# Kernel optimization log

Hardware: AMD Instinct MI355X
Metric: run time of the kernel (lower is better)

The kernel has to match this reference:

```python
import jax, jax.numpy as jnp
import numpy as np

T, C, H, E, TOPK = 8192, 1024, 4096, 8, 2
ALPHA = 0.01


def setup_inputs() -> dict:
    key = jax.random.key(0)
    ks = jax.random.split(key, 10)
    std = 0.01
    return {
        "x": jax.random.normal(ks[0], (T, C), dtype=jnp.float32),
        "gate_w": jax.random.normal(ks[1], (E, C), dtype=jnp.float32) * std,  # nn.init.normal_(std=0.01)
        "wg": jax.random.normal(ks[2], (E, C, H), dtype=jnp.float32) * 0.02,
        "wu": jax.random.normal(ks[3], (E, C, H), dtype=jnp.float32) * 0.02,
        "wd": jax.random.normal(ks[4], (E, H, C), dtype=jnp.float32) * 0.02,
        "swg": jax.random.normal(ks[5], (C, H), dtype=jnp.float32) * 0.02,
        "swu": jax.random.normal(ks[6], (C, H), dtype=jnp.float32) * 0.02,
        "swd": jax.random.normal(ks[7], (H, C), dtype=jnp.float32) * 0.02,
        "shared_scale": jnp.ones((1,), dtype=jnp.float32) * 0.5,
    }


def _swiglu(h, g, u, d):
    # SwiGLU FFN: W_down( silu(W_gate x) * W_up x )
    return (jax.nn.silu(h @ g) * (h @ u)) @ d


def reference(x, gate_w, wg, wu, wd, swg, swu, swd, shared_scale):
    # ---- gate (top-k softmax routing) ----
    logits = x @ gate_w.T                       # [T, E]
    scores = jax.nn.softmax(logits, axis=-1)    # [T, E]
    topk_w, topk_idx = jax.lax.top_k(scores, TOPK)
    topk_w = topk_w / jnp.sum(topk_w, axis=-1, keepdims=True)

    # per-token combine weight for each expert: sum_k w_k * [idx_k == e]  -> [T, E]
    comb = jnp.zeros((x.shape[0], E), dtype=x.dtype)
    comb = comb.at[jnp.arange(x.shape[0])[:, None], topk_idx].add(topk_w)

    # ---- routed experts (dispatch-FFN-combine, expressed as masked dense combine) ----
    y = jnp.zeros_like(x)
    for e in range(E):  # fixed small expert count
        y = y + comb[:, e:e + 1] * _swiglu(x, wg[e], wu[e], wd[e])

    # ---- shared expert ----
    y = y + shared_scale * _swiglu(x, swg, swu, swd)

    # ---- load-balancing aux loss (training mode) ----
    onehot = jax.nn.one_hot(topk_idx.reshape(-1), E, dtype=x.dtype)  # [T*K, E]
    ce = onehot.mean(axis=0)
    fi = ce * E
    Pi = scores.mean(axis=0)
    aux_loss = jnp.sum(Pi * fi) * ALPHA
    return y, aux_loss
```

## Files before the change

kernel.cpp:

```cpp
#include <hip/hip_runtime.h>
#include <hip/hip_bf16.h>
#include <stdint.h>

#define T_TOK 8192
#define CDIM  1024
#define HDIM  4096
#define NEXP  8
#define TOPK_ 2
#define GT_MAX 72
#define UT_MAX 104
#define GROWS_MAX (GT_MAX * 256)

typedef __attribute__((ext_vector_type(8))) short short8;
typedef __attribute__((ext_vector_type(4))) float f32x4;

__device__ __forceinline__ void gload16(const short* g, short* l) {
  __builtin_amdgcn_global_load_lds(
      (const __attribute__((address_space(1))) unsigned int*)(g),
      (__attribute__((address_space(3))) unsigned int*)(l), 16, 0, 0);
}

__global__ __launch_bounds__(256) void gate_kernel(
    const float* __restrict__ x, const float* __restrict__ gw,
    int* __restrict__ tokinfo, float* __restrict__ tokw,
    int* __restrict__ bcnt, float* __restrict__ spart)
{
  const int wid = threadIdx.x >> 6, lane = threadIdx.x & 63;
  const int t = blockIdx.x * 4 + wid;
  float acc[NEXP];
#pragma unroll
  for (int e = 0; e < NEXP; ++e) acc[e] = 0.f;
  const float4* xr = (const float4*)x + (size_t)t * (CDIM / 4);
  const float4* gw4 = (const float4*)gw;
#pragma unroll
  for (int i = 0; i < CDIM / 256; ++i) {
    const float4 xv = xr[lane + 64 * i];
#pragma unroll
    for (int e = 0; e < NEXP; ++e) {
      const float4 gv = gw4[e * (CDIM / 4) + lane + 64 * i];
      acc[e] += xv.x * gv.x + xv.y * gv.y + xv.z * gv.z + xv.w * gv.w;
    }
  }
#pragma unroll
  for (int off = 32; off > 0; off >>= 1) {
#pragma unroll
    for (int e = 0; e < NEXP; ++e) acc[e] += __shfl_xor(acc[e], off);
  }
  float mx = acc[0];
#pragma unroll
  for (int e = 1; e < NEXP; ++e) mx = fmaxf(mx, acc[e]);
  float p[NEXP]; float s = 0.f;
#pragma unroll
  for (int e = 0; e < NEXP; ++e) { p[e] = __expf(acc[e] - mx); s += p[e]; }
  const float inv = 1.f / s;
#pragma unroll
  for (int e = 0; e < NEXP; ++e) p[e] *= inv;
  float v0 = p[0]; int i0 = 0;
#pragma unroll
  for (int e = 1; e < NEXP; ++e) if (p[e] > v0) { v0 = p[e]; i0 = e; }
  float v1 = -1.f; int i1 = 0;
#pragma unroll
  for (int e = 0; e < NEXP; ++e) if (e != i0 && p[e] > v1) { v1 = p[e]; i1 = e; }

  __shared__ float sp[4][NEXP];
  __shared__ int   se[4][2];
  __shared__ float swt[4][2];
  if (lane == 0) {
#pragma unroll
    for (int e = 0; e < NEXP; ++e) sp[wid][e] = p[e];
    const float wn = 1.f / (v0 + v1);
    se[wid][0] = i0; se[wid][1] = i1;
    swt[wid][0] = v0 * wn; swt[wid][1] = v1 * wn;
  }
  __syncthreads();
  if (threadIdx.x == 0) {
    int cnt[NEXP];
#pragma unroll
    for (int e = 0; e < NEXP; ++e) cnt[e] = 0;
#pragma unroll
    for (int tt = 0; tt < 4; ++tt) {
      const int e0 = se[tt][0], e1 = se[tt][1];
      const int r0 = cnt[e0]++; const int r1 = cnt[e1]++;
      tokinfo[blockIdx.x * 4 + tt] = e0 | (e1 << 3) | (r0 << 6) | (r1 << 10);
      ((float2*)tokw)[blockIdx.x * 4 + tt] = make_float2(swt[tt][0], swt[tt][1]);
    }
#pragma unroll
    for (int e = 0; e < NEXP; ++e) bcnt[blockIdx.x * NEXP + e] = cnt[e];
  }
  if (threadIdx.x < NEXP)
    spart[blockIdx.x * NEXP + threadIdx.x] =
        sp[0][threadIdx.x] + sp[1][threadIdx.x] + sp[2][threadIdx.x] + sp[3][threadIdx.x];
}

__global__ __launch_bounds__(512) void scan_kernel(
    const int* __restrict__ bcnt, int* __restrict__ boff, int* __restrict__ ecnt,
    const float* __restrict__ spart, float* __restrict__ aux_out,
    int* __restrict__ pad_off, int* __restrict__ tile_map, int* __restrict__ ntiles)
{
  const int w = threadIdx.x >> 6, l = threadIdx.x & 63;
  int run = 0;
#pragma unroll 4
  for (int c = 0; c < (T_TOK / 4) / 64; ++c) {
    const int b = c * 64 + l;
    const int v = bcnt[b * NEXP + w];
    int sc = v;
#pragma unroll
    for (int off = 1; off < 64; off <<= 1) {
      const int t = __shfl_up(sc, off);
      if (l >= off) sc += t;
    }
    boff[b * NEXP + w] = run + sc - v;
    run += __shfl(sc, 63);
  }
  if (l == 0) ecnt[w] = run;
  float fs = 0.f;
  for (int c = 0; c < (T_TOK / 4) / 64; ++c) fs += spart[(c * 64 + l) * NEXP + w];
#pragma unroll
  for (int off = 32; off > 0; off >>= 1) fs += __shfl_xor(fs, off);
  __shared__ float pis[NEXP];
  __shared__ int cs[NEXP];
  if (l == 0) { pis[w] = fs; cs[w] = run; }
  __syncthreads();
  if (threadIdx.x == 0) {
    float aux = 0.f;
#pragma unroll
    for (int e = 0; e < NEXP; ++e) {
      const float Pi = pis[e] / (float)T_TOK;
      const float ce = (float)cs[e] / (float)(T_TOK * TOPK_);
      aux += Pi * ce * (float)NEXP;
    }
    aux_out[0] = aux * 0.01f;
    ecnt[8] = T_TOK;
    int acc = 0, nt = 0;
    for (int e = 0; e < NEXP; ++e) {
      pad_off[e] = acc;
      const int te = (cs[e] + 255) >> 8;
      for (int t = 0; t < te; ++t) { tile_map[nt] = e | ((t * 256) << 4); ++nt; }
      acc += te * 256;
    }
    ntiles[0] = nt;
    for (int t = 0; t < T_TOK / 256; ++t) { tile_map[nt] = 8 | ((t * 256) << 4); ++nt; }
    ntiles[1] = nt;
  }
}

__global__ __launch_bounds__(256) void scatter_kernel(
    const int* __restrict__ tokinfo, const float* __restrict__ tokw,
    const int* __restrict__ boff, const int* __restrict__ pad_off,
    int* __restrict__ grows, float* __restrict__ gww, int2* __restrict__ tokpos)
{
  const int t = blockIdx.x * 256 + threadIdx.x;
  const int info = tokinfo[t];
  const int e0 = info & 7, e1 = (info >> 3) & 7;
  const int r0 = (info >> 6) & 15, r1 = (info >> 10) & 15;
  const int b = t >> 2;
  const float2 wv = ((const float2*)tokw)[t];
  const int g0 = pad_off[e0] + boff[b * NEXP + e0] + r0;
  grows[g0] = t; gww[g0] = wv.x;
  const int g1 = pad_off[e1] + boff[b * NEXP + e1] + r1;
  grows[g1] = t; gww[g1] = wv.y;
  tokpos[t] = make_int2(g0, g1);
}

__global__ __launch_bounds__(256) void cvt_x_kernel(const float* __restrict__ x,
                                                    __hip_bfloat16* __restrict__ xb)
{
  const int i = blockIdx.x * 256 + threadIdx.x;
  const float4 v = ((const float4*)x)[i];
  union { __hip_bfloat16 h[4]; uint2 u; } o;
  o.h[0] = __float2bfloat16(v.x); o.h[1] = __float2bfloat16(v.y);
  o.h[2] = __float2bfloat16(v.z); o.h[3] = __float2bfloat16(v.w);
  ((uint2*)xb)[i] = o.u;
}

struct TD { const float* src; __hip_bfloat16* dst; int N; int nsh; int M; };
struct TB { TD d[27]; };
__global__ __launch_bounds__(256) void tbatch_kernel(TB tb)
{
  const int m = blockIdx.x >> 12;
  const int t = blockIdx.x & 4095;
  const TD td = tb.d[m];
  const int n0 = (t & ((1 << td.nsh) - 1)) << 5;
  const int m0 = (t >> td.nsh) << 5;
  __shared__ float tile[32][33];
  const int tx = threadIdx.x & 31, ty = threadIdx.x >> 5;
#pragma unroll
  for (int i = 0; i < 4; ++i)
    tile[ty + 8 * i][tx] = td.src[(size_t)(m0 + ty + 8 * i) * td.N + n0 + tx];
  __syncthreads();
#pragma unroll
  for (int i = 0; i < 4; ++i)
    td.dst[(size_t)(n0 + ty + 8 * i) * td.M + m0 + tx] = __float2bfloat16(tile[tx][ty + 8 * i]);
}

__global__ __launch_bounds__(512, 2) void gemm1_pipe_kernel(
    const __hip_bfloat16* __restrict__ Abase,
    const __hip_bfloat16* __restrict__ B0mat, const __hip_bfloat16* __restrict__ B1mat,
    __hip_bfloat16* __restrict__ midout,
    const int* __restrict__ rowlist, const int* __restrict__ ecnt,
    const int* __restrict__ tile_map, const int* __restrict__ ntiles,
    int mode, int tile_base)
{
  constexpr int K = CDIM;
  constexpr int NT = 32;
  __shared__ __align__(16) short lds[65536];

  int ti = blockIdx.y + tile_base;
  if (mode == 2) ti += ntiles[0];
  const int hi = (mode == 1) ? ntiles[0] : ntiles[1];
  if (ti >= hi) return;
  const int tm = tile_map[ti];
  const int e = tm & 15, rb = tm >> 4;
  const int rows_valid = ecnt[e] - rb;
  const int gbmid = (int)blockIdx.y * 256;
  const int glist = ti * 256;

  const int t = threadIdx.x, l = t & 63, w = t >> 6;
  const int sr = t >> 2;
  const int csrc = (t & 3) ^ ((t >> 3) & 3);
  const int n0 = blockIdx.x * 128;

  int r0g, r1g;
  if (e == 8) { r0g = rb + sr; r1g = rb + 128 + sr; }
  else {
    const int c0 = sr < rows_valid ? sr : rows_valid - 1;
    const int c1 = (128 + sr) < rows_valid ? (128 + sr) : rows_valid - 1;
    r0g = rowlist[glist + c0]; r1g = rowlist[glist + c1];
  }
  const short* pA0 = (const short*)Abase + (size_t)r0g * K + csrc * 8;
  const short* pA1 = (const short*)Abase + (size_t)r1g * K + csrc * 8;
  const int br0 = sr, br1 = 128 + sr;
  const int s0 = (br0 >> 4) & 1, s1 = (br1 >> 4) & 1;
  const int h0 = n0 + (br0 >> 5) * 16 + (br0 & 15);
  const int h1 = n0 + (br1 >> 5) * 16 + (br1 & 15);
  const short* pB0 = (const short*)(s0 ? B1mat : B0mat) + (size_t)e * CDIM * HDIM + (size_t)h0 * K + csrc * 8;
  const short* pB1 = (const short*)(s1 ? B1mat : B0mat) + (size_t)e * CDIM * HDIM + (size_t)h1 * K + csrc * 8;

  short* dstA = lds + w * 512;
  short* dstB = lds + 32768 + w * 512;

  const int wr = w >> 2, wc = w & 3;
  const int chunk = (((l >> 4) ^ ((l >> 1) & 3)) << 3);
  const int afb = wr * 4096 + (l & 15) * 32 + chunk;
  const int bfb = 32768 + (wc >> 1) * 4096 + ((wc & 1) * 64 + (l & 15)) * 32 + chunk;

  f32x4 acc[8][4];
#pragma unroll
  for (int i = 0; i < 8; ++i)
#pragma unroll
    for (int j = 0; j < 4; ++j) acc[i][j] = (f32x4){0.f, 0.f, 0.f, 0.f};

#define STAGE_A(q) { const int s8_ = ((q) & 3) * 8192; \
    gload16(pA0 + (q) * 32, dstA + s8_); \
    gload16(pA1 + (q) * 32, dstA + s8_ + 4096); }
#define STAGE_B(q) { const int s8_ = ((q) & 3) * 8192; \
    gload16(pB0 + (q) * 32, dstB + s8_); \
    gload16(pB1 + (q) * 32, dstB + s8_ + 4096); }

  STAGE_A(0) STAGE_B(0) STAGE_A(1) STAGE_B(1)

  short8 af[8], bf[4];
  for (int q = 0; q < NT; ++q) {
    const int s8 = (q & 3) * 8192;
    if (q == NT - 1) {
      asm volatile("s_waitcnt vmcnt(0)\n\ts_barrier" ::: "memory");
    } else {
      asm volatile("s_waitcnt vmcnt(4)\n\ts_barrier" ::: "memory");
    }
    __builtin_amdgcn_sched_barrier(0);
    if (q + 2 < NT) STAGE_A(q + 2)
#pragma unroll
    for (int mi = 0; mi < 4; ++mi) af[mi] = *(const short8*)(lds + s8 + afb + mi * 512);
#pragma unroll
    for (int ni = 0; ni < 4; ++ni) bf[ni] = *(const short8*)(lds + s8 + bfb + ni * 512);
#pragma unroll
    for (int mi = 4; mi < 8; ++mi) af[mi] = *(const short8*)(lds + s8 + afb + mi * 512);
    __builtin_amdgcn_s_setprio(1);
#pragma unroll
    for (int mi = 0; mi < 4; ++mi)
#pragma unroll
      for (int ni = 0; ni < 4; ++ni)
        acc[mi][ni] = __builtin_amdgcn_mfma_f32_16x16x32_bf16(af[mi], bf[ni], acc[mi][ni], 0, 0, 0);
    __builtin_amdgcn_s_setprio(0);
    if (q + 2 < NT) STAGE_B(q + 2)
    __builtin_amdgcn_s_setprio(1);
#pragma unroll
    for (int mi = 4; mi < 8; ++mi)
#pragma unroll
      for (int ni = 0; ni < 4; ++ni)
        acc[mi][ni] = __builtin_amdgcn_mfma_f32_16x16x32_bf16(af[mi], bf[ni], acc[mi][ni], 0, 0, 0);
    __builtin_amdgcn_s_setprio(0);
  }
#undef STAGE_A
#undef STAGE_B

  const int rl = (l >> 4) * 4, cl = l & 15;
#pragma unroll
  for (int mi = 0; mi < 8; ++mi) {
#pragma unroll
    for (int j = 0; j < 4; ++j) {
      const int rlocal = wr * 128 + mi * 16 + rl + j;
      if (rlocal < rows_valid) {
        __hip_bfloat16* mp = midout + (size_t)(gbmid + rlocal) * HDIM;
#pragma unroll
        for (int jj = 0; jj < 2; ++jj) {
          const float g = acc[mi][jj * 2][j], u = acc[mi][jj * 2 + 1][j];
          const float sv = g / (1.f + __expf(-g));
          mp[n0 + (wc * 2 + jj) * 16 + cl] = __float2bfloat16(sv * u);
        }
      }
    }
  }
}

template <int OST>
__global__ __launch_bounds__(512, 1) void gemm2_pipe_kernel(
    const __hip_bfloat16* __restrict__ mid, const __hip_bfloat16* __restrict__ wd9,
    float* __restrict__ mid2, float* __restrict__ y,
    const int* __restrict__ rowlist, const float* __restrict__ roww,
    const int* __restrict__ ecnt, const int* __restrict__ tile_map,
    const int* __restrict__ ntiles, const float* __restrict__ ssc,
    int mode, int tile_base)
{
  constexpr int K = HDIM;
  constexpr int NT = K / 32;
  __shared__ __align__(16) short lds[49152];

  int ti = blockIdx.y + tile_base;
  if (mode == 2) ti += ntiles[0];
  const int hi = (mode == 1) ? ntiles[0] : ntiles[1];
  if (ti >= hi) return;
  const int tm = tile_map[ti];
  const int e = tm & 15, rb = tm >> 4;
  const int rows_valid = ecnt[e] - rb;
  const int gbmid = (int)blockIdx.y * 256;
  const int glist = ti * 256;

  const int t = threadIdx.x, l = t & 63, w = t >> 6;
  const int sr = t >> 2;
  const int csrc = (t & 3) ^ ((t >> 3) & 3);
  const int n0 = blockIdx.x * 128;

  const short* pA0 = (const short*)mid + (size_t)(gbmid + sr) * K + csrc * 8;
  const short* pA1 = pA0 + (size_t)128 * K;
  const short* pB0 = (const short*)wd9 + (size_t)e * CDIM * HDIM + (size_t)(n0 + sr) * K + csrc * 8;

  short* dA = lds + w * 512;
  short* dB = lds + 32768 + w * 512;

  const int wr = w >> 2, wc = w & 3;
  const int chunk = (((l >> 4) ^ ((l >> 1) & 3)) << 3);
  const int afb = wr * 4096 + (l & 15) * 32 + chunk;
  const int bfb = 32768 + (wc * 32 + (l & 15)) * 32 + chunk;

  f32x4 acc[8][2];
#pragma unroll
  for (int i = 0; i < 8; ++i) { acc[i][0] = (f32x4){0.f,0.f,0.f,0.f}; acc[i][1] = (f32x4){0.f,0.f,0.f,0.f}; }

#define S_A(q) { const int o_ = ((q) & 3) * 8192; \
    gload16(pA0 + (size_t)(q) * 32, dA + o_); \
    gload16(pA1 + (size_t)(q) * 32, dA + o_ + 4096); }
#define S_B(q) { const int o_ = ((q) & 3) * 4096; \
    gload16(pB0 + (size_t)(q) * 32, dB + o_); }

  S_A(0) S_B(0) S_A(1) S_B(1)

  short8 af[8], bf[2];
  for (int q = 0; q < NT; ++q) {
    const int sA = (q & 3) * 8192, sB = (q & 3) * 4096;
    if (q == NT - 1) {
      asm volatile("s_waitcnt vmcnt(0)\n\ts_barrier" ::: "memory");
    } else {
      asm volatile("s_waitcnt vmcnt(3)\n\ts_barrier" ::: "memory");
    }
    __builtin_amdgcn_sched_barrier(0);
    if (q + 2 < NT) { S_A(q + 2) S_B(q + 2) }
#pragma unroll
    for (int mi = 0; mi < 8; ++mi) af[mi] = *(const short8*)(lds + sA + afb + mi * 512);
    bf[0] = *(const short8*)(lds + sB + bfb);
    bf[1] = *(const short8*)(lds + sB + bfb + 512);
    __builtin_amdgcn_s_setprio(1);
#pragma unroll
    for (int mi = 0; mi < 8; ++mi) {
      acc[mi][0] = __builtin_amdgcn_mfma_f32_16x16x32_bf16(af[mi], bf[0], acc[mi][0], 0, 0, 0);
      acc[mi][1] = __builtin_amdgcn_mfma_f32_16x16x32_bf16(af[mi], bf[1], acc[mi][1], 0, 0, 0);
    }
    __builtin_amdgcn_s_setprio(0);
  }
#undef S_A
#undef S_B

  const int rl = (l >> 4) * 4, cl = l & 15;
  if (OST) {
#pragma unroll
    for (int mi = 0; mi < 8; ++mi) {
#pragma unroll
      for (int j = 0; j < 4; ++j) {
        const int rlocal = wr * 128 + mi * 16 + rl + j;
        if (rlocal < rows_valid) {
          float* mp = mid2 + (size_t)(glist + rlocal) * CDIM + n0 + wc * 32 + cl;
          mp[0]  = acc[mi][0][j];
          mp[16] = acc[mi][1][j];
        }
      }
    }
  } else {
    const float ss = ssc[0];
#pragma unroll
    for (int mi = 0; mi < 8; ++mi) {
#pragma unroll
      for (int j = 0; j < 4; ++j) {
        const int rlocal = wr * 128 + mi * 16 + rl + j;
        if (rlocal < rows_valid) {
          int tok; float wgt;
          if (e == 8) { tok = rb + rlocal; wgt = ss; }
          else { tok = rowlist[glist + rlocal]; wgt = roww[glist + rlocal]; }
          float* yp = y + (size_t)tok * CDIM + n0 + wc * 32 + cl;
          unsafeAtomicAdd(yp,      wgt * acc[mi][0][j]);
          unsafeAtomicAdd(yp + 16, wgt * acc[mi][1][j]);
        }
      }
    }
  }
}

__global__ __launch_bounds__(256) void combine_kernel(
    const float* __restrict__ mid2, const int* __restrict__ ntiles,
    const int2* __restrict__ tokpos, const float* __restrict__ tokw,
    const float* __restrict__ ssc, float* __restrict__ y)
{
  const int t = blockIdx.x;
  const int c = threadIdx.x * 4;
  const int dbase = ntiles[0] * 256;
  const int2 gp = tokpos[t];
  const float2 wv = ((const float2*)tokw)[t];
  const float ss = ssc[0];
  const float4 d = *(const float4*)(mid2 + (size_t)(dbase + t) * CDIM + c);
  const float4 a = *(const float4*)(mid2 + (size_t)gp.x * CDIM + c);
  const float4 b = *(const float4*)(mid2 + (size_t)gp.y * CDIM + c);
  float4 r;
  r.x = ss * d.x + wv.x * a.x + wv.y * b.x;
  r.y = ss * d.y + wv.x * a.y + wv.y * b.y;
  r.z = ss * d.z + wv.x * a.z + wv.y * b.z;
  r.w = ss * d.w + wv.x * a.w + wv.y * b.w;
  *(float4*)(y + (size_t)t * CDIM + c) = r;
}

extern "C" void kernel_launch(void* const* d_in, const int* in_sizes, int n_in,
                              void* d_out, int out_size, void* d_ws, size_t ws_size,
                              hipStream_t stream)
{
  const float* x   = (const float*)d_in[0];
  const float* gw  = (const float*)d_in[1];
  const float* wg  = (const float*)d_in[2];
  const float* wu  = (const float*)d_in[3];
  const float* wd  = (const float*)d_in[4];
  const float* swg = (const float*)d_in[5];
  const float* swu = (const float*)d_in[6];
  const float* swd = (const float*)d_in[7];
  const float* ssc = (const float*)d_in[8];
  float* y = (float*)d_out;

  auto al = [](size_t v) { return (v + 255) & ~(size_t)255; };
  char* ws = (char*)d_ws;
  size_t off = 0;
  __hip_bfloat16* xb = (__hip_bfloat16*)(ws + off); off += al((size_t)T_TOK * CDIM * 2);
  int*   tokinfo = (int*)(ws + off);   off += al((size_t)T_TOK * 4);
  float* tokw    = (float*)(ws + off); off += al((size_t)T_TOK * 8);
  int2*  tokpos  = (int2*)(ws + off);  off += al((size_t)T_TOK * 8);
  int*   bcnt    = (int*)(ws + off);   off += al((size_t)(T_TOK / 4) * NEXP * 4);
  int*   boffb   = (int*)(ws + off);   off += al((size_t)(T_TOK / 4) * NEXP * 4);
  float* spart   = (float*)(ws + off); off += al((size_t)(T_TOK / 4) * NEXP * 4);
  int*   ecnt    = (int*)(ws + off);   off += 256;
  int*   pad_off = (int*)(ws + off);   off += 256;
  int*   ntiles  = (int*)(ws + off);   off += 256;
  int*   tile_map= (int*)(ws + off);   off += al((size_t)UT_MAX * 4);
  int*   grows   = (int*)(ws + off);   off += al((size_t)GROWS_MAX * 4);
  float* gww     = (float*)(ws + off); off += al((size_t)GROWS_MAX * 4);

  const size_t WMAT = (size_t)CDIM * HDIM;
  __hip_bfloat16* wg9 = (__hip_bfloat16*)(ws + off); off += 9 * WMAT * 2;
  __hip_bfloat16* wu9 = (__hip_bfloat16*)(ws + off); off += 9 * WMAT * 2;
  __hip_bfloat16* wd9 = (__hip_bfloat16*)(ws + off); off += 9 * WMAT * 2;
  __hip_bfloat16* mid = (__hip_bfloat16*)(ws + off);
  const size_t mid_avail = (ws_size > off) ? (ws_size - off) : 0;
  const size_t TILE_B = (size_t)256 * HDIM * 2;
  const size_t MIDB   = (size_t)UT_MAX * TILE_B;
  const size_t MID2B  = (size_t)UT_MAX * 256 * CDIM * 4;

  gate_kernel<<<T_TOK / 4, 256, 0, stream>>>(x, gw, tokinfo, tokw, bcnt, spart);
  scan_kernel<<<1, 512, 0, stream>>>(bcnt, boffb, ecnt, spart, y + (size_t)T_TOK * CDIM,
                                     pad_off, tile_map, ntiles);
  scatter_kernel<<<T_TOK / 256, 256, 0, stream>>>(tokinfo, tokw, boffb, pad_off,
                                                  grows, gww, tokpos);
  cvt_x_kernel<<<T_TOK * CDIM / 4 / 256, 256, 0, stream>>>(x, xb);

  TB tb;
  for (int e = 0; e < 8; ++e) {
    tb.d[e]      = TD{wg + e * WMAT, wg9 + e * WMAT, HDIM, 7, CDIM};
    tb.d[8 + e]  = TD{wu + e * WMAT, wu9 + e * WMAT, HDIM, 7, CDIM};
    tb.d[16 + e] = TD{wd + e * WMAT, wd9 + e * WMAT, CDIM, 5, HDIM};
  }
  tb.d[24] = TD{swg, wg9 + 8 * WMAT, HDIM, 7, CDIM};
  tb.d[25] = TD{swu, wu9 + 8 * WMAT, HDIM, 7, CDIM};
  tb.d[26] = TD{swd, wd9 + 8 * WMAT, CDIM, 5, HDIM};
  tbatch_kernel<<<27 * 4096, 256, 0, stream>>>(tb);

  if (mid_avail >= MIDB + MID2B) {
    float* mid2 = (float*)((char*)mid + MIDB);
    gemm1_pipe_kernel<<<dim3(HDIM / 128, UT_MAX), 512, 0, stream>>>(
        xb, wg9, wu9, mid, grows, ecnt, tile_map, ntiles, 0, 0);
    gemm2_pipe_kernel<1><<<dim3(CDIM / 128, UT_MAX), 512, 0, stream>>>(
        mid, wd9, mid2, nullptr, grows, gww, ecnt, tile_map, ntiles, ssc, 0, 0);
    combine_kernel<<<T_TOK, 256, 0, stream>>>(mid2, ntiles, tokpos, tokw, ssc, y);
  } else if (mid_avail >= MIDB) {
    hipMemsetAsync(y, 0, (size_t)T_TOK * CDIM * sizeof(float), stream);
    gemm1_pipe_kernel<<<dim3(HDIM / 128, UT_MAX), 512, 0, stream>>>(
        xb, wg9, wu9, mid, grows, ecnt, tile_map, ntiles, 0, 0);
    gemm2_pipe_kernel<0><<<dim3(CDIM / 128, UT_MAX), 512, 0, stream>>>(
        mid, wd9, nullptr, y, grows, gww, ecnt, tile_map, ntiles, ssc, 0, 0);
  } else {
    hipMemsetAsync(y, 0, (size_t)T_TOK * CDIM * sizeof(float), stream);
    int CH = (int)(mid_avail / TILE_B);
    if (CH < 1) CH = 1;
    for (int c0 = 0; c0 < GT_MAX; c0 += CH) {
      const int g = (GT_MAX - c0) < CH ? (GT_MAX - c0) : CH;
      gemm1_pipe_kernel<<<dim3(HDIM / 128, g), 512, 0, stream>>>(
          xb, wg9, wu9, mid, grows, ecnt, tile_map, ntiles, 1, c0);
      gemm2_pipe_kernel<0><<<dim3(CDIM / 128, g), 512, 0, stream>>>(
          mid, wd9, nullptr, y, grows, gww, ecnt, tile_map, ntiles, ssc, 1, c0);
    }
    for (int c0 = 0; c0 < 32; c0 += CH) {
      const int g = (32 - c0) < CH ? (32 - c0) : CH;
      gemm1_pipe_kernel<<<dim3(HDIM / 128, g), 512, 0, stream>>>(
          xb, wg9, wu9, mid, grows, ecnt, tile_map, ntiles, 2, c0);
      gemm2_pipe_kernel<0><<<dim3(CDIM / 128, g), 512, 0, stream>>>(
          mid, wd9, nullptr, y, grows, gww, ecnt, tile_map, ntiles, ssc, 2, c0);
    }
  }
}
```

Measured before the change: 1.006 ms.

## Fuse x bf16 conversion into gate; rework GEMM pipelines to BK=64 double-buffer

Result: no change. 1.014 ms (+0.8%).

```diff
diff --git a/kernel.cpp b/kernel.cpp
--- a/kernel.cpp
+++ b/kernel.cpp
@@ -23,7 +23,8 @@
 __global__ __launch_bounds__(256) void gate_kernel(
     const float* __restrict__ x, const float* __restrict__ gw,
     int* __restrict__ tokinfo, float* __restrict__ tokw,
-    int* __restrict__ bcnt, float* __restrict__ spart)
+    int* __restrict__ bcnt, float* __restrict__ spart,
+    __hip_bfloat16* __restrict__ xb)
 {
   const int wid = threadIdx.x >> 6, lane = threadIdx.x & 63;
   const int t = blockIdx.x * 4 + wid;
@@ -32,9 +33,14 @@
   for (int e = 0; e < NEXP; ++e) acc[e] = 0.f;
   const float4* xr = (const float4*)x + (size_t)t * (CDIM / 4);
   const float4* gw4 = (const float4*)gw;
+  uint2* xbo = (uint2*)(xb + (size_t)t * CDIM);
 #pragma unroll
   for (int i = 0; i < CDIM / 256; ++i) {
     const float4 xv = xr[lane + 64 * i];
+    union { __hip_bfloat16 h[4]; uint2 u; } o;
+    o.h[0] = __float2bfloat16(xv.x); o.h[1] = __float2bfloat16(xv.y);
+    o.h[2] = __float2bfloat16(xv.z); o.h[3] = __float2bfloat16(xv.w);
+    xbo[lane + 64 * i] = o.u;
 #pragma unroll
     for (int e = 0; e < NEXP; ++e) {
       const float4 gv = gw4[e * (CDIM / 4) + lane + 64 * i];
@@ -162,17 +168,6 @@
   tokpos[t] = make_int2(g0, g1);
 }
 
-__global__ __launch_bounds__(256) void cvt_x_kernel(const float* __restrict__ x,
-                                                    __hip_bfloat16* __restrict__ xb)
-{
-  const int i = blockIdx.x * 256 + threadIdx.x;
-  const float4 v = ((const float4*)x)[i];
-  union { __hip_bfloat16 h[4]; uint2 u; } o;
-  o.h[0] = __float2bfloat16(v.x); o.h[1] = __float2bfloat16(v.y);
-  o.h[2] = __float2bfloat16(v.z); o.h[3] = __float2bfloat16(v.w);
-  ((uint2*)xb)[i] = o.u;
-}
-
 struct TD { const float* src; __hip_bfloat16* dst; int N; int nsh; int M; };
 struct TB { TD d[27]; };
 __global__ __launch_bounds__(256) void tbatch_kernel(TB tb)
@@ -202,7 +197,7 @@
     int mode, int tile_base)
 {
   constexpr int K = CDIM;
-  constexpr int NT = 32;
+  constexpr int NTL = K / 64;
   __shared__ __align__(16) short lds[65536];
 
   int ti = blockIdx.y + tile_base;
@@ -216,33 +211,30 @@
   const int glist = ti * 256;
 
   const int t = threadIdx.x, l = t & 63, w = t >> 6;
-  const int sr = t >> 2;
-  const int csrc = (t & 3) ^ ((t >> 3) & 3);
-  const int n0 = blockIdx.x * 128;
-
-  int r0g, r1g;
-  if (e == 8) { r0g = rb + sr; r1g = rb + 128 + sr; }
-  else {
-    const int c0 = sr < rows_valid ? sr : rows_valid - 1;
-    const int c1 = (128 + sr) < rows_valid ? (128 + sr) : rows_valid - 1;
-    r0g = rowlist[glist + c0]; r1g = rowlist[glist + c1];
-  }
-  const short* pA0 = (const short*)Abase + (size_t)r0g * K + csrc * 8;
-  const short* pA1 = (const short*)Abase + (size_t)r1g * K + csrc * 8;
-  const int br0 = sr, br1 = 128 + sr;
-  const int s0 = (br0 >> 4) & 1, s1 = (br1 >> 4) & 1;
-  const int h0 = n0 + (br0 >> 5) * 16 + (br0 & 15);
-  const int h1 = n0 + (br1 >> 5) * 16 + (br1 & 15);
-  const short* pB0 = (const short*)(s0 ? B1mat : B0mat) + (size_t)e * CDIM * HDIM + (size_t)h0 * K + csrc * 8;
-  const short* pB1 = (const short*)(s1 ? B1mat : B0mat) + (size_t)e * CDIM * HDIM + (size_t)h1 * K + csrc * 8;
-
-  short* dstA = lds + w * 512;
-  short* dstB = lds + 32768 + w * 512;
-
   const int wr = w >> 2, wc = w & 3;
-  const int chunk = (((l >> 4) ^ ((l >> 1) & 3)) << 3);
-  const int afb = wr * 4096 + (l & 15) * 32 + chunk;
-  const int bfb = 32768 + (wc >> 1) * 4096 + ((wc & 1) * 64 + (l & 15)) * 32 + chunk;
+  const int n0h = blockIdx.x * 128;
+
+  const int rbase = w * 8 + (l >> 3);
+  const int ksrc = ((l & 7) ^ ((l >> 3) & 7)) * 8;
+  const short* pA[4]; const short* pB[4];
+#pragma unroll
+  for (int j = 0; j < 4; ++j) {
+    const int rl_ = j * 64 + rbase;
+    int rg;
+    if (e == 8) rg = rb + rl_;
+    else { const int c = rl_ < rows_valid ? rl_ : rows_valid - 1; rg = rowlist[glist + c]; }
+    pA[j] = (const short*)Abase + (size_t)rg * K + ksrc;
+    const int s = (rl_ >> 4) & 1;
+    const int h = n0h + (rl_ >> 5) * 16 + (rl_ & 15);
+    pB[j] = (const short*)(s ? B1mat : B0mat) + (size_t)e * CDIM * HDIM + (size_t)h * K + ksrc;
+  }
+  const int dst0 = w * 512 + l * 8;
+
+#define STG(tt) { const int bb_ = ((tt) & 1) * 16384; \
+    gload16(pA[0] + (tt) * 64, lds + bb_ + dst0);          gload16(pB[0] + (tt) * 64, lds + 32768 + bb_ + dst0); \
+    gload16(pA[1] + (tt) * 64, lds + bb_ + 4096 + dst0);   gload16(pB[1] + (tt) * 64, lds + 32768 + bb_ + 4096 + dst0); \
+    gload16(pA[2] + (tt) * 64, lds + bb_ + 8192 + dst0);   gload16(pB[2] + (tt) * 64, lds + 32768 + bb_ + 8192 + dst0); \
+    gload16(pA[3] + (tt) * 64, lds + bb_ + 12288 + dst0);  gload16(pB[3] + (tt) * 64, lds + 32768 + bb_ + 12288 + dst0); }
 
   f32x4 acc[8][4];
 #pragma unroll
@@ -250,49 +242,33 @@
 #pragma unroll
     for (int j = 0; j < 4; ++j) acc[i][j] = (f32x4){0.f, 0.f, 0.f, 0.f};
 
-#define STAGE_A(q) { const int s8_ = ((q) & 3) * 8192; \
-    gload16(pA0 + (q) * 32, dstA + s8_); \
-    gload16(pA1 + (q) * 32, dstA + s8_ + 4096); }
-#define STAGE_B(q) { const int s8_ = ((q) & 3) * 8192; \
-    gload16(pB0 + (q) * 32, dstB + s8_); \
-    gload16(pB1 + (q) * 32, dstB + s8_ + 4096); }
-
-  STAGE_A(0) STAGE_B(0) STAGE_A(1) STAGE_B(1)
-
-  short8 af[8], bf[4];
-  for (int q = 0; q < NT; ++q) {
-    const int s8 = (q & 3) * 8192;
-    if (q == NT - 1) {
-      asm volatile("s_waitcnt vmcnt(0)\n\ts_barrier" ::: "memory");
-    } else {
-      asm volatile("s_waitcnt vmcnt(4)\n\ts_barrier" ::: "memory");
-    }
+  STG(0)
+  for (int tt = 0; tt < NTL; ++tt) {
+    asm volatile("s_waitcnt vmcnt(0)\n\ts_barrier" ::: "memory");
     __builtin_amdgcn_sched_barrier(0);
-    if (q + 2 < NT) STAGE_A(q + 2)
-#pragma unroll
-    for (int mi = 0; mi < 4; ++mi) af[mi] = *(const short8*)(lds + s8 + afb + mi * 512);
-#pragma unroll
-    for (int ni = 0; ni < 4; ++ni) bf[ni] = *(const short8*)(lds + s8 + bfb + ni * 512);
-#pragma unroll
-    for (int mi = 4; mi < 8; ++mi) af[mi] = *(const short8*)(lds + s8 + afb + mi * 512);
-    __builtin_amdgcn_s_setprio(1);
-#pragma unroll
-    for (int mi = 0; mi < 4; ++mi)
+    if (tt + 1 < NTL) STG(tt + 1)
+    const int ab = (tt & 1) * 16384, bb = 32768 + (tt & 1) * 16384;
+#pragma unroll
+    for (int ks = 0; ks < 2; ++ks) {
+      short8 af[8], bf[4];
+      const int cb = ks * 4 + (l >> 4);
+      const int csw = (cb ^ (l & 7)) * 8;
+#pragma unroll
+      for (int mi = 0; mi < 8; ++mi)
+        af[mi] = *(const short8*)(lds + ab + (wr * 128 + mi * 16 + (l & 15)) * 64 + csw);
 #pragma unroll
       for (int ni = 0; ni < 4; ++ni)
-        acc[mi][ni] = __builtin_amdgcn_mfma_f32_16x16x32_bf16(af[mi], bf[ni], acc[mi][ni], 0, 0, 0);
-    __builtin_amdgcn_s_setprio(0);
-    if (q + 2 < NT) STAGE_B(q + 2)
-    __builtin_amdgcn_s_setprio(1);
-#pragma unroll
-    for (int mi = 4; mi < 8; ++mi)
-#pragma unroll
-      for (int ni = 0; ni < 4; ++ni)
-        acc[mi][ni] = __builtin_amdgcn_mfma_f32_16x16x32_bf16(af[mi], bf[ni], acc[mi][ni], 0, 0, 0);
-    __builtin_amdgcn_s_setprio(0);
-  }
-#undef STAGE_A
-#undef STAGE_B
+        bf[ni] = *(const short8*)(lds + bb + (wc * 64 + ni * 16 + (l & 15)) * 64 + csw);
+      __builtin_amdgcn_s_setprio(1);
+#pragma unroll
+      for (int mi = 0; mi < 8; ++mi)
+#pragma unroll
+        for (int ni = 0; ni < 4; ++ni)
+          acc[mi][ni] = __builtin_amdgcn_mfma_f32_16x16x32_bf16(af[mi], bf[ni], acc[mi][ni], 0, 0, 0);
+      __builtin_amdgcn_s_setprio(0);
+    }
+  }
+#undef STG
 
   const int rl = (l >> 4) * 4, cl = l & 15;
 #pragma unroll
@@ -306,7 +282,7 @@
         for (int jj = 0; jj < 2; ++jj) {
           const float g = acc[mi][jj * 2][j], u = acc[mi][jj * 2 + 1][j];
           const float sv = g / (1.f + __expf(-g));
-          mp[n0 + (wc * 2 + jj) * 16 + cl] = __float2bfloat16(sv * u);
+          mp[n0h + (wc * 2 + jj) * 16 + cl] = __float2bfloat16(sv * u);
         }
       }
     }
@@ -314,7 +290,7 @@
 }
 
 template <int OST>
-__global__ __launch_bounds__(512, 1) void gemm2_pipe_kernel(
+__global__ __launch_bounds__(512, 2) void gemm2_pipe_kernel(
     const __hip_bfloat16* __restrict__ mid, const __hip_bfloat16* __restrict__ wd9,
     float* __restrict__ mid2, float* __restrict__ y,
     const int* __restrict__ rowlist, const float* __restrict__ roww,
@@ -323,7 +299,7 @@
     int mode, int tile_base)
 {
   constexpr int K = HDIM;
-  constexpr int NT = K / 32;
+  constexpr int NTL = K / 64;
   __shared__ __align__(16) short lds[49152];
 
   int ti = blockIdx.y + tile_base;
@@ -337,87 +313,91 @@
   const int glist = ti * 256;
 
   const int t = threadIdx.x, l = t & 63, w = t >> 6;
-  const int sr = t >> 2;
-  const int csrc = (t & 3) ^ ((t >> 3) & 3);
+  const int wr = w & 3, wc = w >> 2;
   const int n0 = blockIdx.x * 128;
 
-  const short* pA0 = (const short*)mid + (size_t)(gbmid + sr) * K + csrc * 8;
-  const short* pA1 = pA0 + (size_t)128 * K;
-  const short* pB0 = (const short*)wd9 + (size_t)e * CDIM * HDIM + (size_t)(n0 + sr) * K + csrc * 8;
-
-  short* dA = lds + w * 512;
-  short* dB = lds + 32768 + w * 512;
-
-  const int wr = w >> 2, wc = w & 3;
-  const int chunk = (((l >> 4) ^ ((l >> 1) & 3)) << 3);
-  const int afb = wr * 4096 + (l & 15) * 32 + chunk;
-  const int bfb = 32768 + (wc * 32 + (l & 15)) * 32 + chunk;
-
-  f32x4 acc[8][2];
-#pragma unroll
-  for (int i = 0; i < 8; ++i) { acc[i][0] = (f32x4){0.f,0.f,0.f,0.f}; acc[i][1] = (f32x4){0.f,0.f,0.f,0.f}; }
-
-#define S_A(q) { const int o_ = ((q) & 3) * 8192; \
-    gload16(pA0 + (size_t)(q) * 32, dA + o_); \
-    gload16(pA1 + (size_t)(q) * 32, dA + o_ + 4096); }
-#define S_B(q) { const int o_ = ((q) & 3) * 4096; \
-    gload16(pB0 + (size_t)(q) * 32, dB + o_); }
-
-  S_A(0) S_B(0) S_A(1) S_B(1)
-
-  short8 af[8], bf[2];
-  for (int q = 0; q < NT; ++q) {
-    const int sA = (q & 3) * 8192, sB = (q & 3) * 4096;
-    if (q == NT - 1) {
-      asm volatile("s_waitcnt vmcnt(0)\n\ts_barrier" ::: "memory");
-    } else {
-      asm volatile("s_waitcnt vmcnt(3)\n\ts_barrier" ::: "memory");
-    }
+  const int rbase = w * 8 + (l >> 3);
+  const int ksrc = ((l & 7) ^ ((l >> 3) & 7)) * 8;
+  const short* pA[4]; const short* pB[2];
+#pragma unroll
+  for (int j = 0; j < 4; ++j)
+    pA[j] = (const short*)mid + (size_t)(gbmid + j * 64 + rbase) * K + ksrc;
+#pragma unroll
+  for (int j = 0; j < 2; ++j)
+    pB[j] = (const short*)wd9 + (size_t)e * CDIM * HDIM + (size_t)(n0 + j * 64 + rbase) * K + ksrc;
+  const int dst0 = w * 512 + l * 8;
+
+#define STG2(tt) { const int ab_ = ((tt) & 1) * 16384, bb_ = 32768 + ((tt) & 1) * 8192; \
+    gload16(pA[0] + (size_t)(tt) * 64, lds + ab_ + dst0); \
+    gload16(pA[1] + (size_t)(tt) * 64, lds + ab_ + 4096 + dst0); \
+    gload16(pA[2] + (size_t)(tt) * 64, lds + ab_ + 8192 + dst0); \
+    gload16(pA[3] + (size_t)(tt) * 64, lds + ab_ + 12288 + dst0); \
+    gload16(pB[0] + (size_t)(tt) * 64, lds + bb_ + dst0); \
+    gload16(pB[1] + (size_t)(tt) * 64, lds + bb_ + 4096 + dst0); }
+
+  f32x4 acc[4][4];
+#pragma unroll
+  for (int i = 0; i < 4; ++i)
+#pragma unroll
+    for (int j = 0; j < 4; ++j) acc[i][j] = (f32x4){0.f, 0.f, 0.f, 0.f};
+
+  STG2(0)
+  for (int tt = 0; tt < NTL; ++tt) {
+    asm volatile("s_waitcnt vmcnt(0)\n\ts_barrier" ::: "memory");
     __builtin_amdgcn_sched_barrier(0);
-    if (q + 2 < NT) { S_A(q + 2) S_B(q + 2) }
-#pragma unroll
-    for (int mi = 0; mi < 8; ++mi) af[mi] = *(const short8*)(lds + sA + afb + mi * 512);
-    bf[0] = *(const short8*)(lds + sB + bfb);
-    bf[1] = *(const short8*)(lds + sB + bfb + 512);
-    __builtin_amdgcn_s_setprio(1);
-#pragma unroll
-    for (int mi = 0; mi < 8; ++mi) {
-      acc[mi][0] = __builtin_amdgcn_mfma_f32_16x16x32_bf16(af[mi], bf[0], acc[mi][0], 0, 0, 0);
-      acc[mi][1] = __builtin_amdgcn_mfma_f32_16x16x32_bf16(af[mi], bf[1], acc[mi][1], 0, 0, 0);
-    }
-    __builtin_amdgcn_s_setprio(0);
-  }
-#undef S_A
-#undef S_B
+    if (tt + 1 < NTL) STG2(tt + 1)
+    const int ab = (tt & 1) * 16384, bb = 32768 + (tt & 1) * 8192;
+#pragma unroll
+    for (int ks = 0; ks < 2; ++ks) {
+      short8 af[4], bf[4];
+      const int cb = ks * 4 + (l >> 4);
+      const int csw = (cb ^ (l & 7)) * 8;
+#pragma unroll
+      for (int mi = 0; mi < 4; ++mi)
+        af[mi] = *(const short8*)(lds + ab + (wr * 64 + mi * 16 + (l & 15)) * 64 + csw);
+#pragma unroll
+      for (int ni = 0; ni < 4; ++ni)
+        bf[ni] = *(const short8*)(lds + bb + (wc * 64 + ni * 16 + (l & 15)) * 64 + csw);
+      __builtin_amdgcn_s_setprio(1);
+#pragma unroll
+      for (int mi = 0; mi < 4; ++mi)
+#pragma unroll
+        for (int ni = 0; ni < 4; ++ni)
+          acc[mi][ni] = __builtin_amdgcn_mfma_f32_16x16x32_bf16(af[mi], bf[ni], acc[mi][ni], 0, 0, 0);
+      __builtin_amdgcn_s_setprio(0);
+    }
+  }
+#undef STG2
 
   const int rl = (l >> 4) * 4, cl = l & 15;
   if (OST) {
 #pragma unroll
-    for (int mi = 0; mi < 8; ++mi) {
+    for (int mi = 0; mi < 4; ++mi) {
 #pragma unroll
       for (int j = 0; j < 4; ++j) {
-        const int rlocal = wr * 128 + mi * 16 + rl + j;
+        const int rlocal = wr * 64 + mi * 16 + rl + j;
         if (rlocal < rows_valid) {
-          float* mp = mid2 + (size_t)(glist + rlocal) * CDIM + n0 + wc * 32 + cl;
-          mp[0]  = acc[mi][0][j];
-          mp[16] = acc[mi][1][j];
+          float* mp = mid2 + (size_t)(glist + rlocal) * CDIM + n0 + wc * 64 + cl;
+#pragma unroll
+          for (int ni = 0; ni < 4; ++ni) mp[ni * 16] = acc[mi][ni][j];
         }
       }
     }
   } else {
     const float ss = ssc[0];
 #pragma unroll
-    for (int mi = 0; mi < 8; ++mi) {
+    for (int mi = 0; mi < 4; ++mi) {
 #pragma unroll
       for (int j = 0; j < 4; ++j) {
-        const int rlocal = wr * 128 + mi * 16 + rl + j;
+        const int rlocal = wr * 64 + mi * 16 + rl + j;
         if (rlocal < rows_valid) {
           int tok; float wgt;
           if (e == 8) { tok = rb + rlocal; wgt = ss; }
           else { tok = rowlist[glist + rlocal]; wgt = roww[glist + rlocal]; }
-          float* yp = y + (size_t)tok * CDIM + n0 + wc * 32 + cl;
-          unsafeAtomicAdd(yp,      wgt * acc[mi][0][j]);
-          unsafeAtomicAdd(yp + 16, wgt * acc[mi][1][j]);
+          float* yp = y + (size_t)tok * CDIM + n0 + wc * 64 + cl;
+#pragma unroll
+          for (int ni = 0; ni < 4; ++ni)
+            unsafeAtomicAdd(yp + ni * 16, wgt * acc[mi][ni][j]);
         }
       }
     }
@@ -488,12 +468,11 @@
   const size_t MIDB   = (size_t)UT_MAX * TILE_B;
   const size_t MID2B  = (size_t)UT_MAX * 256 * CDIM * 4;
 
-  gate_kernel<<<T_TOK / 4, 256, 0, stream>>>(x, gw, tokinfo, tokw, bcnt, spart);
+  gate_kernel<<<T_TOK / 4, 256, 0, stream>>>(x, gw, tokinfo, tokw, bcnt, spart, xb);
   scan_kernel<<<1, 512, 0, stream>>>(bcnt, boffb, ecnt, spart, y + (size_t)T_TOK * CDIM,
                                      pad_off, tile_map, ntiles);
   scatter_kernel<<<T_TOK / 256, 256, 0, stream>>>(tokinfo, tokw, boffb, pad_off,
                                                   grows, gww, tokpos);
-  cvt_x_kernel<<<T_TOK * CDIM / 4 / 256, 256, 0, stream>>>(x, xb);
 
   TB tb;
   for (int e = 0; e < 8; ++e) {
```
